# Optimization experiments

Measured on AMD Instinct MI355X. Metric: run time of the kernel, lower is better.

Reference implementation:

```python
import jax, jax.numpy as jnp
import numpy as np
from jax import lax

SEQ_LEN = 256
BATCH = 512
N_INPUTS = 3
N_LAYERS = 2
HIDDEN = 512
TD_ACT = SEQ_LEN  # required: fc1 is Linear(seq_len, 20) applied to td output
N_OUTPUTS = 2


def _lstm_layer(x, h0, c0, Wih, Whh, bih, bhh):
    # x: [S, B, I]; h0, c0: [B, H]; Wih: [4H, I]; Whh: [4H, H]
    def step(carry, xt):
        h, c = carry
        gates = xt @ Wih.T + bih + h @ Whh.T + bhh  # [B, 4H]
        i, f, g, o = jnp.split(gates, 4, axis=-1)
        i = jax.nn.sigmoid(i)
        f = jax.nn.sigmoid(f)
        g = jnp.tanh(g)
        o = jax.nn.sigmoid(o)
        c = f * c + i * g
        h = o * jnp.tanh(c)
        return (h, c), h

    (hT, cT), ys = lax.scan(step, (h0, c0), x)
    return ys, hT, cT


def setup_inputs() -> dict:
    key = jax.random.key(0)
    ks = jax.random.split(key, 16)
    s = 1.0 / np.sqrt(HIDDEN)
    u = lambda k, shape: jax.random.uniform(k, shape, jnp.float32, -s, s)
    return {
        "x": jax.random.normal(ks[0], (SEQ_LEN, BATCH, N_INPUTS), jnp.float32),
        "h0": jax.random.normal(ks[1], (N_LAYERS, BATCH, HIDDEN), jnp.float32),
        "c0": jax.random.normal(ks[2], (N_LAYERS, BATCH, HIDDEN), jnp.float32),
        "Wih0": u(ks[3], (4 * HIDDEN, N_INPUTS)),
        "Whh0": u(ks[4], (4 * HIDDEN, HIDDEN)),
        "bih0": u(ks[5], (4 * HIDDEN,)),
        "bhh0": u(ks[6], (4 * HIDDEN,)),
        "Wih1": u(ks[7], (4 * HIDDEN, HIDDEN)),
        "Whh1": u(ks[8], (4 * HIDDEN, HIDDEN)),
        "bih1": u(ks[9], (4 * HIDDEN,)),
        "bhh1": u(ks[10], (4 * HIDDEN,)),
        "Wtd": u(ks[11], (TD_ACT, 2 * HIDDEN)),
        "btd": u(ks[12], (TD_ACT,)),
        "Wfc1": u(ks[13], (20, SEQ_LEN)),
        "bfc1": jnp.zeros((20,), jnp.float32),
        "Wfc2": u(ks[14], (N_OUTPUTS, 20)),
        "bfc2": jnp.zeros((N_OUTPUTS,), jnp.float32),
    }


def reference(x, h0, c0, Wih0, Whh0, bih0, bhh0, Wih1, Whh1, bih1, bhh1,
              Wtd, btd, Wfc1, bfc1, Wfc2, bfc2):
    # layer 0
    y0, h0T, _ = _lstm_layer(x, h0[0], c0[0], Wih0, Whh0, bih0, bhh0)
    # layer 1
    y1, h1T, _ = _lstm_layer(y0, h0[1], c0[1], Wih1, Whh1, bih1, bhh1)
    # hn[-2] = h0T, hn[-1] = h1T
    cat = jnp.concatenate([h0T, h1T], axis=1)  # [B, 2H]
    td = cat @ Wtd.T + btd                     # [B, TD_ACT == SEQ_LEN]
    fc1 = jax.nn.relu(td @ Wfc1.T + bfc1)      # [B, 20] (dropout p=0 is identity)
    out = fc1 @ Wfc2.T + bfc2                  # [B, 2]
    return out
```

## Files before the change

kernel.cpp:

```cpp
#include <hip/hip_runtime.h>
#include <math.h>

#define BB 512
#define HH 512
#define SS 256
#define XD0 3
#define TDN 256
#define FC1N 20
#define OUTN 2
#define TM 32
#define TN 32
#define TK 32
#define NBLK 256

typedef __attribute__((ext_vector_type(8))) short short8;
typedef __attribute__((ext_vector_type(4))) short short4v;
typedef __attribute__((ext_vector_type(4))) float f32x4;
typedef unsigned long long u64;

__device__ __forceinline__ unsigned short bf16_rne(float f) {
    unsigned u = __float_as_uint(f);
    u += 0x7FFFu + ((u >> 16) & 1u);
    return (unsigned short)(u >> 16);
}
__device__ __forceinline__ float bf16_to_f(unsigned short h) {
    return __uint_as_float(((unsigned)h) << 16);
}
__device__ __forceinline__ float sigmoid_(float x) { return 1.0f / (1.0f + __expf(-x)); }
__device__ __forceinline__ float tanh_(float x) {
    float e = __expf(2.0f * x);
    return 1.0f - 2.0f / (e + 1.0f);
}

__device__ __forceinline__ short8 cload8(const short* p) {
    u64 a = __hip_atomic_load((const u64*)p,     __ATOMIC_RELAXED, __HIP_MEMORY_SCOPE_AGENT);
    u64 b = __hip_atomic_load((const u64*)p + 1, __ATOMIC_RELAXED, __HIP_MEMORY_SCOPE_AGENT);
    union { u64 q[2]; short8 v; } u;
    u.q[0] = a; u.q[1] = b;
    return u.v;
}
__device__ __forceinline__ void cstore4(short* p, short4v v) {
    u64 q; __builtin_memcpy(&q, &v, 8);
    __hip_atomic_store((u64*)p, q, __ATOMIC_RELAXED, __HIP_MEMORY_SCOPE_AGENT);
}

__global__ __launch_bounds__(256)
void cvt_wfrag(const float* __restrict__ W, short* __restrict__ hi, short* __restrict__ lo)
{
    int idx = blockIdx.x * 256 + threadIdx.x;
    int l   = idx & 63;
    int kt  = (idx >> 6) & 15;
    int g   = (idx >> 10) & 3;
    int jt  = idx >> 12;
    int row = g * HH + jt * 16 + (l & 15);
    int col = kt * 32 + (l >> 4) * 8;
    size_t src = (size_t)row * HH + col;
    size_t dst = (size_t)idx * 8;
    #pragma unroll
    for (int e = 0; e < 8; ++e) {
        float v = W[src + e];
        unsigned short h = bf16_rne(v);
        hi[dst + e] = (short)h;
        lo[dst + e] = (short)bf16_rne(v - bf16_to_f(h));
    }
}

__global__ __launch_bounds__(256)
void cvt_hfrag(const float* __restrict__ Hsrc, short* __restrict__ hi, short* __restrict__ lo)
{
    int idx = blockIdx.x * 256 + threadIdx.x;
    int l  = idx & 63;
    int kt = (idx >> 6) & 15;
    int rt = idx >> 10;
    int r = rt * 16 + (l & 15);
    int k = kt * 32 + (l >> 4) * 8;
    size_t src = (size_t)r * HH + k;
    size_t dst = (size_t)idx * 8;
    #pragma unroll
    for (int e = 0; e < 8; ++e) {
        float v = Hsrc[src + e];
        unsigned short h = bf16_rne(v);
        hi[dst + e] = (short)h;
        lo[dst + e] = (short)bf16_rne(v - bf16_to_f(h));
    }
}

__global__ void zero_sync(unsigned* s) { s[threadIdx.x] = 0u; }

__device__ __forceinline__ void grid_barrier(unsigned* sync, int p, int bid)
{
    __syncthreads();
    if (threadIdx.x == 0) {
        const int g = bid & 7;
        unsigned a = __hip_atomic_fetch_add(&sync[g * 32], 1u,
                        __ATOMIC_RELAXED, __HIP_MEMORY_SCOPE_AGENT);
        if (a == (unsigned)((NBLK / 8) * (p + 1) - 1)) {
            unsigned r = __hip_atomic_fetch_add(&sync[256], 1u,
                            __ATOMIC_RELAXED, __HIP_MEMORY_SCOPE_AGENT);
            if (r == (unsigned)(8 * (p + 1) - 1)) {
                __hip_atomic_store(&sync[320], (unsigned)(p + 1),
                                   __ATOMIC_RELAXED, __HIP_MEMORY_SCOPE_AGENT);
            }
        }
        while (__hip_atomic_load(&sync[320], __ATOMIC_RELAXED,
                                 __HIP_MEMORY_SCOPE_AGENT) < (unsigned)(p + 1)) {
            __builtin_amdgcn_s_sleep(2);
        }
    }
    __syncthreads();
}

template<int LAYER>
__device__ __forceinline__ void reduce_epilogue(
    f32x4 (&acc)[4][4], float (*quad)[4096],
    int kh, int l, int tid, int jt, int rblk, int p,
    const float* __restrict__ sbias,
    const float* __restrict__ swin,
    const float* __restrict__ cinit,
    f32x4& cstate,
    short* __restrict__ hfh, short* __restrict__ hfl,
    float* __restrict__ Hf,
    const float* __restrict__ x)
{
    if (kh >= 4) {
        #pragma unroll
        for (int rt = 0; rt < 4; ++rt)
            #pragma unroll
            for (int g = 0; g < 4; ++g)
                #pragma unroll
                for (int q = 0; q < 4; ++q)
                    quad[kh - 4][(g*64 + rt*16 + (l>>4)*4 + q)*16 + (l&15)] = acc[rt][g][q];
    }
    __syncthreads();
    if (kh < 4) {
        #pragma unroll
        for (int rt = 0; rt < 4; ++rt)
            #pragma unroll
            for (int g = 0; g < 4; ++g)
                #pragma unroll
                for (int q = 0; q < 4; ++q)
                    acc[rt][g][q] += quad[kh][(g*64 + rt*16 + (l>>4)*4 + q)*16 + (l&15)];
    }
    __syncthreads();
    if (kh == 2 || kh == 3) {
        #pragma unroll
        for (int rt = 0; rt < 4; ++rt)
            #pragma unroll
            for (int g = 0; g < 4; ++g)
                #pragma unroll
                for (int q = 0; q < 4; ++q)
                    quad[kh][(g*64 + rt*16 + (l>>4)*4 + q)*16 + (l&15)] = acc[rt][g][q];
    }
    __syncthreads();
    if (kh == 0 || kh == 1) {
        #pragma unroll
        for (int rt = 0; rt < 4; ++rt)
            #pragma unroll
            for (int g = 0; g < 4; ++g)
                #pragma unroll
                for (int q = 0; q < 4; ++q)
                    acc[rt][g][q] += quad[kh + 2][(g*64 + rt*16 + (l>>4)*4 + q)*16 + (l&15)];
        if (kh == 1) {
            #pragma unroll
            for (int rt = 0; rt < 4; ++rt)
                #pragma unroll
                for (int g = 0; g < 4; ++g)
                    #pragma unroll
                    for (int q = 0; q < 4; ++q)
                        quad[1][(g*64 + rt*16 + (l>>4)*4 + q)*16 + (l&15)] = acc[rt][g][q];
        }
    }
    __syncthreads();
    if (kh == 0) {
        #pragma unroll
        for (int rt = 0; rt < 4; ++rt)
            #pragma unroll
            for (int g = 0; g < 4; ++g) {
                #pragma unroll
                for (int q = 0; q < 4; ++q) {
                    acc[rt][g][q] += quad[1][(g*64 + rt*16 + (l>>4)*4 + q)*16 + (l&15)];
                    quad[0][(g*64 + rt*16 + (l>>4)*4 + q)*16 + (l&15)] = acc[rt][g][q];
                }
            }
    }
    __syncthreads();

    if (tid < 256) {
        const int rl = tid >> 2;
        const int jl = (tid & 3) * 4;
        const int r  = rblk * 64 + rl;
        const int j  = jt * 16 + jl;
        f32x4 gv[4];
        #pragma unroll
        for (int g = 0; g < 4; ++g) {
            gv[g] = *(const f32x4*)&quad[0][(g*64 + rl)*16 + jl];
            f32x4 bv = *(const f32x4*)&sbias[g*16 + jl];
            #pragma unroll
            for (int q = 0; q < 4; ++q) gv[g][q] += bv[q];
        }
        if (LAYER == 0) {
            const float x0 = x[(size_t)p * BB * XD0 + r * XD0 + 0];
            const float x1 = x[(size_t)p * BB * XD0 + r * XD0 + 1];
            const float x2 = x[(size_t)p * BB * XD0 + r * XD0 + 2];
            #pragma unroll
            for (int g = 0; g < 4; ++g)
                #pragma unroll
                for (int e = 0; e < 4; ++e) {
                    const float* wr_ = &swin[(g*16 + jl + e) * 3];
                    gv[g][e] += x0 * wr_[0] + x1 * wr_[1] + x2 * wr_[2];
                }
        }
        f32x4 cv = cstate;
        if (cinit != nullptr) cv = *(const f32x4*)&cinit[(size_t)r * HH + j];
        float hn[4];
        #pragma unroll
        for (int e = 0; e < 4; ++e) {
            float I = sigmoid_(gv[0][e]);
            float F = sigmoid_(gv[1][e]);
            float G = tanh_(gv[2][e]);
            float O = sigmoid_(gv[3][e]);
            float cn = F * cv[e] + I * G;
            cv[e] = cn;
            hn[e] = O * tanh_(cn);
        }
        cstate = cv;
        const int ktj   = j >> 5;
        const int lanew = (r & 15) | (((j & 31) >> 3) << 4);
        const int e0    = j & 7;
        const int rtg   = r >> 4;
        size_t hoff = ((((size_t)rtg)*16 + ktj)*64 + lanew)*8 + e0;
        short4v hhi, hlo;
        #pragma unroll
        for (int e = 0; e < 4; ++e) {
            unsigned short hb = bf16_rne(hn[e]);
            hhi[e] = (short)hb;
            hlo[e] = (short)bf16_rne(hn[e] - bf16_to_f(hb));
        }
        cstore4(&hfh[hoff], hhi);
        cstore4(&hfl[hoff], hlo);
        if (Hf != nullptr) {
            f32x4 hv;
            #pragma unroll
            for (int e = 0; e < 4; ++e) hv[e] = hn[e];
            *(f32x4*)&Hf[(size_t)r * HH + j] = hv;
        }
    }
    __syncthreads();
}

__global__ __launch_bounds__(512, 2)
void lstm_persist(
    const short* __restrict__ W0h, const short* __restrict__ W0l,
    const short* __restrict__ W1h, const short* __restrict__ W1l,
    const short* __restrict__ WIh, const short* __restrict__ WIl,
    const float* __restrict__ Wih0, const float* __restrict__ x,
    const float* __restrict__ bih0, const float* __restrict__ bhh0,
    const float* __restrict__ bih1, const float* __restrict__ bhh1,
    const float* __restrict__ c0in,
    short* __restrict__ h0fh0, short* __restrict__ h0fl0,
    short* __restrict__ h0fh1, short* __restrict__ h0fl1,
    short* __restrict__ h1fh0, short* __restrict__ h1fl0,
    short* __restrict__ h1fh1, short* __restrict__ h1fl1,
    float* __restrict__ H0f, float* __restrict__ H1f,
    unsigned* __restrict__ sync)
{
    __shared__ float quad[4][4096];
    __shared__ __align__(16) float sb[2][64];
    __shared__ float swin[192];

    const int tid  = threadIdx.x;
    const int kh   = tid >> 6;
    const int l    = tid & 63;
    const int bid  = blockIdx.x;
    const int jt   = bid & 31;
    const int rblk = bid >> 5;

    if (tid < 128) {
        const int L = tid >> 6;
        const int gj = tid & 63;
        const int g = gj >> 4, jl = gj & 15;
        const int j = jt * 16 + jl;
        const float* bi = L ? bih1 : bih0;
        const float* bh = L ? bhh1 : bhh0;
        sb[L][gj] = bi[g * HH + j] + bh[g * HH + j];
    } else if (tid < 320) {
        const int q = tid - 128;
        const int gj = q / 3, d = q - gj * 3;
        const int g = gj >> 4, jl = gj & 15;
        const int j = jt * 16 + jl;
        swin[q] = Wih0[(size_t)(g * HH + j) * XD0 + d];
    }

    short8 b0h[2][4];
    short8 b1h[4][4];
    #pragma unroll
    for (int kk = 0; kk < 2; ++kk)
        #pragma unroll
        for (int g = 0; g < 4; ++g)
            b0h[kk][g] = *(const short8*)&W0h[((((size_t)jt*4 + g)*16 + (kh + kk*8))*64 + l)*8];
    #pragma unroll
    for (int kk = 0; kk < 4; ++kk)
        #pragma unroll
        for (int g = 0; g < 4; ++g) {
            const short* Wh = (kk < 2) ? W1h : WIh;
            const int kt = kh + (kk & 1) * 8;
            b1h[kk][g] = *(const short8*)&Wh[((((size_t)jt*4 + g)*16 + kt)*64 + l)*8];
        }

    f32x4 c0reg, c1reg;
    #pragma unroll
    for (int e = 0; e < 4; ++e) { c0reg[e] = 0.0f; c1reg[e] = 0.0f; }

    __syncthreads();

    for (int p = 0; p <= SS; ++p) {
        const int par = p & 1;
        if (p < SS) {
            const short* Ah = par ? h0fh1 : h0fh0;
            const short* Al = par ? h0fl1 : h0fl0;
            f32x4 acc[4][4];
            #pragma unroll
            for (int rt = 0; rt < 4; ++rt)
                #pragma unroll
                for (int g = 0; g < 4; ++g)
                    #pragma unroll
                    for (int q = 0; q < 4; ++q) acc[rt][g][q] = 0.0f;
            #pragma unroll
            for (int kk = 0; kk < 2; ++kk) {
                const int kt = kh + kk * 8;
                short8 bl[4];
                #pragma unroll
                for (int g = 0; g < 4; ++g)
                    bl[g] = *(const short8*)&W0l[((((size_t)jt*4 + g)*16 + kt)*64 + l)*8];
                #pragma unroll
                for (int rt = 0; rt < 4; ++rt) {
                    const size_t ab = ((((size_t)(rblk*4 + rt))*16 + kt)*64 + l)*8;
                    short8 ah = cload8(&Ah[ab]);
                    short8 al = cload8(&Al[ab]);
                    #pragma unroll
                    for (int g = 0; g < 4; ++g) {
                        acc[rt][g] = __builtin_amdgcn_mfma_f32_16x16x32_bf16(ah, b0h[kk][g], acc[rt][g], 0,0,0);
                        acc[rt][g] = __builtin_amdgcn_mfma_f32_16x16x32_bf16(ah, bl[g],      acc[rt][g], 0,0,0);
                        acc[rt][g] = __builtin_amdgcn_mfma_f32_16x16x32_bf16(al, b0h[kk][g], acc[rt][g], 0,0,0);
                    }
                }
            }
            reduce_epilogue<0>(acc, quad, kh, l, tid, jt, rblk, p,
                               sb[0], swin,
                               (p == 0) ? c0in : nullptr, c0reg,
                               par ? h0fh0 : h0fh1, par ? h0fl0 : h0fl1,
                               (p == SS - 1) ? H0f : nullptr, x);
        }
        if (p >= 1) {
            const short* A1h = par ? h1fh1 : h1fh0;
            const short* A1l = par ? h1fl1 : h1fl0;
            const short* Y0h = par ? h0fh1 : h0fh0;
            const short* Y0l = par ? h0fl1 : h0fl0;
            f32x4 acc[4][4];
            #pragma unroll
            for (int rt = 0; rt < 4; ++rt)
                #pragma unroll
                for (int g = 0; g < 4; ++g)
                    #pragma unroll
                    for (int q = 0; q < 4; ++q) acc[rt][g][q] = 0.0f;
            #pragma unroll
            for (int kk = 0; kk < 4; ++kk) {
                const int kt = kh + (kk & 1) * 8;
                const short* Ah = (kk < 2) ? A1h : Y0h;
                const short* Al = (kk < 2) ? A1l : Y0l;
                const short* Wl = (kk < 2) ? W1l : WIl;
                short8 bl[4];
                #pragma unroll
                for (int g = 0; g < 4; ++g)
                    bl[g] = *(const short8*)&Wl[((((size_t)jt*4 + g)*16 + kt)*64 + l)*8];
                #pragma unroll
                for (int rt = 0; rt < 4; ++rt) {
                    const size_t ab = ((((size_t)(rblk*4 + rt))*16 + kt)*64 + l)*8;
                    short8 ah = cload8(&Ah[ab]);
                    short8 al = cload8(&Al[ab]);
                    #pragma unroll
                    for (int g = 0; g < 4; ++g) {
                        acc[rt][g] = __builtin_amdgcn_mfma_f32_16x16x32_bf16(ah, b1h[kk][g], acc[rt][g], 0,0,0);
                        acc[rt][g] = __builtin_amdgcn_mfma_f32_16x16x32_bf16(ah, bl[g],      acc[rt][g], 0,0,0);
                        acc[rt][g] = __builtin_amdgcn_mfma_f32_16x16x32_bf16(al, b1h[kk][g], acc[rt][g], 0,0,0);
                    }
                }
            }
            reduce_epilogue<1>(acc, quad, kh, l, tid, jt, rblk, p,
                               sb[1], swin,
                               (p == 1) ? (c0in + (size_t)BB*HH) : nullptr, c1reg,
                               par ? h1fh0 : h1fh1, par ? h1fl0 : h1fl1,
                               (p == SS) ? H1f : nullptr, x);
        }
        grid_barrier(sync, p, bid);
    }
}

__global__ __launch_bounds__(256)
void td_kernel(const float* __restrict__ h0T, const float* __restrict__ h1T,
               const float* __restrict__ Wtd, const float* __restrict__ btd,
               float* __restrict__ td)
{
    __shared__ float a_lds[TM][TK + 1];
    __shared__ float b_lds[TN][TK + 1];
    const int t = threadIdx.x;
    const int nl = t & 31;
    const int mq = t >> 5;
    const int n0 = blockIdx.x * TN;
    const int m0 = blockIdx.y * TM;
    float acc[4] = {0.f, 0.f, 0.f, 0.f};

    for (int k0 = 0; k0 < 2 * HH; k0 += TK) {
        const float* src = (k0 < HH) ? h0T : h1T;
        int kb = k0 & (HH - 1);
        #pragma unroll
        for (int i = 0; i < (TM * TK) / 256; ++i) {
            int idx = t + i * 256;
            int r = idx >> 5, kk = idx & 31;
            a_lds[r][kk] = src[(size_t)(m0 + r) * HH + kb + kk];
        }
        #pragma unroll
        for (int i = 0; i < (TN * TK) / 256; ++i) {
            int idx = t + i * 256;
            int jn = idx >> 5, kk = idx & 31;
            b_lds[jn][kk] = Wtd[(size_t)(n0 + jn) * (2 * HH) + k0 + kk];
        }
        __syncthreads();
        #pragma unroll
        for (int kk = 0; kk < TK; ++kk) {
            float bv = b_lds[nl][kk];
            #pragma unroll
            for (int rr = 0; rr < 4; ++rr)
                acc[rr] = fmaf(a_lds[mq * 4 + rr][kk], bv, acc[rr]);
        }
        __syncthreads();
    }
    #pragma unroll
    for (int rr = 0; rr < 4; ++rr)
        td[(size_t)(m0 + mq * 4 + rr) * TDN + n0 + nl] = acc[rr] + btd[n0 + nl];
}

__global__ __launch_bounds__(256)
void fc_kernel(const float* __restrict__ td,
               const float* __restrict__ Wfc1, const float* __restrict__ bfc1,
               const float* __restrict__ Wfc2, const float* __restrict__ bfc2,
               float* __restrict__ out)
{
    __shared__ float td_lds[32][TDN];
    __shared__ float f1_lds[32][FC1N];
    const int t = threadIdx.x;
    const int r0 = blockIdx.x * 32;

    #pragma unroll
    for (int i = 0; i < (32 * TDN) / 256; ++i) {
        int idx = t + i * 256;
        int r = idx >> 8, k = idx & 255;
        td_lds[r][k] = td[(size_t)(r0 + r) * TDN + k];
    }
    __syncthreads();

    for (int idx = t; idx < 32 * FC1N; idx += 256) {
        int r = idx / FC1N, o = idx % FC1N;
        float s = bfc1[o];
        for (int k = 0; k < TDN; ++k) s = fmaf(td_lds[r][k], Wfc1[o * TDN + k], s);
        f1_lds[r][o] = fmaxf(s, 0.0f);
    }
    __syncthreads();

    for (int idx = t; idx < 32 * OUTN; idx += 256) {
        int r = idx / OUTN, o = idx % OUTN;
        float s = bfc2[o];
        for (int k = 0; k < FC1N; ++k) s = fmaf(f1_lds[r][k], Wfc2[o * FC1N + k], s);
        out[(size_t)(r0 + r) * OUTN + o] = s;
    }
}

extern "C" void kernel_launch(void* const* d_in, const int* in_sizes, int n_in,
                              void* d_out, int out_size, void* d_ws, size_t ws_size,
                              hipStream_t stream)
{
    const float* x    = (const float*)d_in[0];
    const float* h0   = (const float*)d_in[1];
    const float* c0   = (const float*)d_in[2];
    const float* Wih0 = (const float*)d_in[3];
    const float* Whh0 = (const float*)d_in[4];
    const float* bih0 = (const float*)d_in[5];
    const float* bhh0 = (const float*)d_in[6];
    const float* Wih1 = (const float*)d_in[7];
    const float* Whh1 = (const float*)d_in[8];
    const float* bih1 = (const float*)d_in[9];
    const float* bhh1 = (const float*)d_in[10];
    const float* Wtd  = (const float*)d_in[11];
    const float* btd  = (const float*)d_in[12];
    const float* Wfc1 = (const float*)d_in[13];
    const float* bfc1 = (const float*)d_in[14];
    const float* Wfc2 = (const float*)d_in[15];
    const float* bfc2 = (const float*)d_in[16];
    float* out = (float*)d_out;

    const size_t WSZ = (size_t)4 * HH * HH;
    const size_t HFR = (size_t)32 * 16 * 64 * 8;
    const size_t HSZ = (size_t)BB * HH;

    char* pp = (char*)d_ws;
    short* W0h = (short*)pp; pp += WSZ * 2;
    short* W0l = (short*)pp; pp += WSZ * 2;
    short* W1h = (short*)pp; pp += WSZ * 2;
    short* W1l = (short*)pp; pp += WSZ * 2;
    short* WIh = (short*)pp; pp += WSZ * 2;
    short* WIl = (short*)pp; pp += WSZ * 2;
    short* h0fh0 = (short*)pp; pp += HFR * 2;
    short* h0fl0 = (short*)pp; pp += HFR * 2;
    short* h0fh1 = (short*)pp; pp += HFR * 2;
    short* h0fl1 = (short*)pp; pp += HFR * 2;
    short* h1fh0 = (short*)pp; pp += HFR * 2;
    short* h1fl0 = (short*)pp; pp += HFR * 2;
    short* h1fh1 = (short*)pp; pp += HFR * 2;
    short* h1fl1 = (short*)pp; pp += HFR * 2;
    float* H0f = (float*)pp; pp += HSZ * 4;
    float* H1f = (float*)pp; pp += HSZ * 4;
    float* TD  = (float*)pp; pp += (size_t)BB * TDN * 4;
    unsigned* sync = (unsigned*)pp; pp += 512 * 4;

    cvt_wfrag<<<dim3(512), dim3(256), 0, stream>>>(Whh0, W0h, W0l);
    cvt_wfrag<<<dim3(512), dim3(256), 0, stream>>>(Whh1, W1h, W1l);
    cvt_wfrag<<<dim3(512), dim3(256), 0, stream>>>(Wih1, WIh, WIl);
    cvt_hfrag<<<dim3(128), dim3(256), 0, stream>>>(h0,        h0fh0, h0fl0);
    cvt_hfrag<<<dim3(128), dim3(256), 0, stream>>>(h0 + HSZ,  h1fh1, h1fl1);
    zero_sync<<<dim3(1), dim3(512), 0, stream>>>(sync);

    lstm_persist<<<dim3(NBLK), dim3(512), 0, stream>>>(
        W0h, W0l, W1h, W1l, WIh, WIl,
        Wih0, x, bih0, bhh0, bih1, bhh1, c0,
        h0fh0, h0fl0, h0fh1, h0fl1,
        h1fh0, h1fl0, h1fh1, h1fl1,
        H0f, H1f, sync);

    const dim3 gtd(TDN / TN, BB / TM);
    td_kernel<<<gtd, dim3(256), 0, stream>>>(H0f, H1f, Wtd, btd, TD);
    fc_kernel<<<dim3(BB / 32), dim3(256), 0, stream>>>(TD, Wfc1, bfc1, Wfc2, bfc2, out);

    (void)in_sizes; (void)n_in; (void)out_size; (void)ws_size;
}
```

Baseline: 9.958 ms.

## Map row blocks to XCDs and use per-XCD barriers with non-coherent loads

At launch each block reads its hardware XCD id and takes a slot on that XCD. If every XCD holds exactly 32 blocks, each XCD owns one batch row block (rblk = xcd). Those blocks then sync only with the 32 blocks on their own XCD and exchange h fragments with plain cached loads and stores instead of agent-scope atomics. This is meant to replace the device-wide barrier and cross-XCD coherent traffic with a cheaper local barrier and L2-resident data. It relies on same-XCD L2 coherence for the plain accesses, and falls back to the old global path if the placement check fails.

```diff
diff --git a/kernel.cpp b/kernel.cpp
--- a/kernel.cpp
+++ b/kernel.cpp
@@ -18,6 +18,8 @@
 typedef __attribute__((ext_vector_type(4))) float f32x4;
 typedef unsigned long long u64;
 
+#define SYNC_WORDS 1024
+
 __device__ __forceinline__ unsigned short bf16_rne(float f) {
     unsigned u = __float_as_uint(f);
     u += 0x7FFFu + ((u >> 16) & 1u);
@@ -42,6 +44,15 @@
 __device__ __forceinline__ void cstore4(short* p, short4v v) {
     u64 q; __builtin_memcpy(&q, &v, 8);
     __hip_atomic_store((u64*)p, q, __ATOMIC_RELAXED, __HIP_MEMORY_SCOPE_AGENT);
+}
+
+template<bool COH> __device__ __forceinline__ short8 ald(const short* p) {
+    if constexpr (COH) return cload8(p);
+    else return *(const short8*)p;
+}
+template<bool COH> __device__ __forceinline__ void ast(short* p, short4v v) {
+    if constexpr (COH) cstore4(p, v);
+    else *(short4v*)p = v;
 }
 
 __global__ __launch_bounds__(256)
@@ -85,42 +96,55 @@
     }
 }
 
-__global__ void zero_sync(unsigned* s) { s[threadIdx.x] = 0u; }
-
-__device__ __forceinline__ void grid_barrier(unsigned* sync, int p, int bid)
+__global__ void zero_sync(unsigned* s) { s[blockIdx.x * 256 + threadIdx.x] = 0u; }
+
+template<bool COH>
+__device__ __forceinline__ void phase_barrier(unsigned* sync, int p, int bid, int rblk)
 {
     __syncthreads();
     if (threadIdx.x == 0) {
-        const int g = bid & 7;
-        unsigned a = __hip_atomic_fetch_add(&sync[g * 32], 1u,
-                        __ATOMIC_RELAXED, __HIP_MEMORY_SCOPE_AGENT);
-        if (a == (unsigned)((NBLK / 8) * (p + 1) - 1)) {
-            unsigned r = __hip_atomic_fetch_add(&sync[256], 1u,
+        if constexpr (COH) {
+            const int g = bid & 7;
+            unsigned a = __hip_atomic_fetch_add(&sync[g * 32], 1u,
                             __ATOMIC_RELAXED, __HIP_MEMORY_SCOPE_AGENT);
-            if (r == (unsigned)(8 * (p + 1) - 1)) {
-                __hip_atomic_store(&sync[320], (unsigned)(p + 1),
+            if (a == (unsigned)((NBLK / 8) * (p + 1) - 1)) {
+                unsigned r = __hip_atomic_fetch_add(&sync[256], 1u,
+                                __ATOMIC_RELAXED, __HIP_MEMORY_SCOPE_AGENT);
+                if (r == (unsigned)(8 * (p + 1) - 1)) {
+                    __hip_atomic_store(&sync[320], (unsigned)(p + 1),
+                                       __ATOMIC_RELAXED, __HIP_MEMORY_SCOPE_AGENT);
+                }
+            }
+            while (__hip_atomic_load(&sync[320], __ATOMIC_RELAXED,
+                                     __HIP_MEMORY_SCOPE_AGENT) < (unsigned)(p + 1)) {
+                __builtin_amdgcn_s_sleep(2);
+            }
+        } else {
+            unsigned* cnt = &sync[512 + rblk * 64];
+            unsigned* gen = &sync[512 + rblk * 64 + 32];
+            unsigned a = __hip_atomic_fetch_add(cnt, 1u,
+                            __ATOMIC_RELAXED, __HIP_MEMORY_SCOPE_AGENT);
+            if (a == (unsigned)(32 * (p + 1) - 1)) {
+                __hip_atomic_store(gen, (unsigned)(p + 1),
                                    __ATOMIC_RELAXED, __HIP_MEMORY_SCOPE_AGENT);
             }
-        }
-        while (__hip_atomic_load(&sync[320], __ATOMIC_RELAXED,
-                                 __HIP_MEMORY_SCOPE_AGENT) < (unsigned)(p + 1)) {
-            __builtin_amdgcn_s_sleep(2);
-        }
-    }
-    __syncthreads();
-}
-
-template<int LAYER>
+            while (__hip_atomic_load(gen, __ATOMIC_RELAXED,
+                                     __HIP_MEMORY_SCOPE_AGENT) < (unsigned)(p + 1)) {
+                __builtin_amdgcn_s_sleep(1);
+            }
+        }
+    }
+    __syncthreads();
+}
+
+template<int LAYER, bool COH>
 __device__ __forceinline__ void reduce_epilogue(
     f32x4 (&acc)[4][4], float (*quad)[4096],
     int kh, int l, int tid, int jt, int rblk, int p,
-    const float* __restrict__ sbias,
-    const float* __restrict__ swin,
-    const float* __restrict__ cinit,
-    f32x4& cstate,
+    const float* __restrict__ sbias, const float* __restrict__ swin,
+    const float* __restrict__ cinit, f32x4& cstate,
     short* __restrict__ hfh, short* __restrict__ hfl,
-    float* __restrict__ Hf,
-    const float* __restrict__ x)
+    float* __restrict__ Hf, const float* __restrict__ x)
 {
     if (kh >= 4) {
         #pragma unroll
@@ -236,8 +260,8 @@
             hhi[e] = (short)hb;
             hlo[e] = (short)bf16_rne(hn[e] - bf16_to_f(hb));
         }
-        cstore4(&hfh[hoff], hhi);
-        cstore4(&hfl[hoff], hlo);
+        ast<COH>(&hfh[hoff], hhi);
+        ast<COH>(&hfl[hoff], hlo);
         if (Hf != nullptr) {
             f32x4 hv;
             #pragma unroll
@@ -246,6 +270,145 @@
         }
     }
     __syncthreads();
+}
+
+template<bool COH>
+__device__ __forceinline__ void run_main(
+    int tid, int bid, int rblk, int jt,
+    float (*quad)[4096], float (*sb)[64], float* swin,
+    const short* W0h, const short* W0l,
+    const short* W1h, const short* W1l,
+    const short* WIh, const short* WIl,
+    const float* Wih0, const float* x,
+    const float* bih0, const float* bhh0,
+    const float* bih1, const float* bhh1,
+    const float* c0in,
+    short* h0fh0, short* h0fl0, short* h0fh1, short* h0fl1,
+    short* h1fh0, short* h1fl0, short* h1fh1, short* h1fl1,
+    float* H0f, float* H1f, unsigned* sync)
+{
+    const int kh = tid >> 6;
+    const int l  = tid & 63;
+
+    if (tid < 128) {
+        const int L = tid >> 6;
+        const int gj = tid & 63;
+        const int g = gj >> 4, jl = gj & 15;
+        const int j = jt * 16 + jl;
+        const float* bi = L ? bih1 : bih0;
+        const float* bh = L ? bhh1 : bhh0;
+        sb[L][gj] = bi[g * HH + j] + bh[g * HH + j];
+    } else if (tid < 320) {
+        const int q = tid - 128;
+        const int gj = q / 3, d = q - gj * 3;
+        const int g = gj >> 4, jl = gj & 15;
+        const int j = jt * 16 + jl;
+        swin[q] = Wih0[(size_t)(g * HH + j) * XD0 + d];
+    }
+
+    short8 b0h[2][4];
+    short8 b1h[4][4];
+    #pragma unroll
+    for (int kk = 0; kk < 2; ++kk)
+        #pragma unroll
+        for (int g = 0; g < 4; ++g)
+            b0h[kk][g] = *(const short8*)&W0h[((((size_t)jt*4 + g)*16 + (kh + kk*8))*64 + l)*8];
+    #pragma unroll
+    for (int kk = 0; kk < 4; ++kk)
+        #pragma unroll
+        for (int g = 0; g < 4; ++g) {
+            const short* Wh = (kk < 2) ? W1h : WIh;
+            const int kt = kh + (kk & 1) * 8;
+            b1h[kk][g] = *(const short8*)&Wh[((((size_t)jt*4 + g)*16 + kt)*64 + l)*8];
+        }
+
+    f32x4 c0reg, c1reg;
+    #pragma unroll
+    for (int e = 0; e < 4; ++e) { c0reg[e] = 0.0f; c1reg[e] = 0.0f; }
+
+    __syncthreads();
+
+    for (int p = 0; p <= SS; ++p) {
+        const int par = p & 1;
+        if (p < SS) {
+            const short* Ah = par ? h0fh1 : h0fh0;
+            const short* Al = par ? h0fl1 : h0fl0;
+            f32x4 acc[4][4];
+            #pragma unroll
+            for (int rt = 0; rt < 4; ++rt)
+                #pragma unroll
+                for (int g = 0; g < 4; ++g)
+                    #pragma unroll
+                    for (int q = 0; q < 4; ++q) acc[rt][g][q] = 0.0f;
+            #pragma unroll
+            for (int kk = 0; kk < 2; ++kk) {
+                const int kt = kh + kk * 8;
+                short8 bl[4];
+                #pragma unroll
+                for (int g = 0; g < 4; ++g)
+                    bl[g] = *(const short8*)&W0l[((((size_t)jt*4 + g)*16 + kt)*64 + l)*8];
+                #pragma unroll
+                for (int rt = 0; rt < 4; ++rt) {
+                    const size_t ab = ((((size_t)(rblk*4 + rt))*16 + kt)*64 + l)*8;
+                    short8 ah = ald<COH>(&Ah[ab]);
+                    short8 al = ald<COH>(&Al[ab]);
+                    #pragma unroll
+                    for (int g = 0; g < 4; ++g) {
+                        acc[rt][g] = __builtin_amdgcn_mfma_f32_16x16x32_bf16(ah, b0h[kk][g], acc[rt][g], 0,0,0);
+                        acc[rt][g] = __builtin_amdgcn_mfma_f32_16x16x32_bf16(ah, bl[g],      acc[rt][g], 0,0,0);
+                        acc[rt][g] = __builtin_amdgcn_mfma_f32_16x16x32_bf16(al, b0h[kk][g], acc[rt][g], 0,0,0);
+                    }
+                }
+            }
+            reduce_epilogue<0, COH>(acc, quad, kh, l, tid, jt, rblk, p,
+                               sb[0], swin,
+                               (p == 0) ? c0in : nullptr, c0reg,
+                               par ? h0fh0 : h0fh1, par ? h0fl0 : h0fl1,
+                               (p == SS - 1) ? H0f : nullptr, x);
+        }
+        if (p >= 1) {
+            const short* A1h = par ? h1fh1 : h1fh0;
+            const short* A1l = par ? h1fl1 : h1fl0;
+            const short* Y0h = par ? h0fh1 : h0fh0;
+            const short* Y0l = par ? h0fl1 : h0fl0;
+            f32x4 acc[4][4];
+            #pragma unroll
+            for (int rt = 0; rt < 4; ++rt)
+                #pragma unroll
+                for (int g = 0; g < 4; ++g)
+                    #pragma unroll
+                    for (int q = 0; q < 4; ++q) acc[rt][g][q] = 0.0f;
+            #pragma unroll
+            for (int kk = 0; kk < 4; ++kk) {
+                const int kt = kh + (kk & 1) * 8;
+                const short* Ah = (kk < 2) ? A1h : Y0h;
+                const short* Al = (kk < 2) ? A1l : Y0l;
+                const short* Wl = (kk < 2) ? W1l : WIl;
+                short8 bl[4];
+                #pragma unroll
+                for (int g = 0; g < 4; ++g)
+                    bl[g] = *(const short8*)&Wl[((((size_t)jt*4 + g)*16 + kt)*64 + l)*8];
+                #pragma unroll
+                for (int rt = 0; rt < 4; ++rt) {
+                    const size_t ab = ((((size_t)(rblk*4 + rt))*16 + kt)*64 + l)*8;
+                    short8 ah = ald<COH>(&Ah[ab]);
+                    short8 al = ald<COH>(&Al[ab]);
+                    #pragma unroll
+                    for (int g = 0; g < 4; ++g) {
+                        acc[rt][g] = __builtin_amdgcn_mfma_f32_16x16x32_bf16(ah, b1h[kk][g], acc[rt][g], 0,0,0);
+                        acc[rt][g] = __builtin_amdgcn_mfma_f32_16x16x32_bf16(ah, bl[g],      acc[rt][g], 0,0,0);
+                        acc[rt][g] = __builtin_amdgcn_mfma_f32_16x16x32_bf16(al, b1h[kk][g], acc[rt][g], 0,0,0);
+                    }
+                }
+            }
+            reduce_epilogue<1, COH>(acc, quad, kh, l, tid, jt, rblk, p,
+                               sb[1], swin,
+                               (p == 1) ? (c0in + (size_t)BB*HH) : nullptr, c1reg,
+                               par ? h1fh0 : h1fh1, par ? h1fl0 : h1fl1,
+                               (p == SS) ? H1f : nullptr, x);
+        }
+        phase_barrier<COH>(sync, p, bid, rblk);
+    }
 }
 
 __global__ __launch_bounds__(512, 2)
@@ -267,132 +430,49 @@
     __shared__ float quad[4][4096];
     __shared__ __align__(16) float sb[2][64];
     __shared__ float swin[192];
-
-    const int tid  = threadIdx.x;
-    const int kh   = tid >> 6;
-    const int l    = tid & 63;
-    const int bid  = blockIdx.x;
-    const int jt   = bid & 31;
-    const int rblk = bid >> 5;
-
-    if (tid < 128) {
-        const int L = tid >> 6;
-        const int gj = tid & 63;
-        const int g = gj >> 4, jl = gj & 15;
-        const int j = jt * 16 + jl;
-        const float* bi = L ? bih1 : bih0;
-        const float* bh = L ? bhh1 : bhh0;
-        sb[L][gj] = bi[g * HH + j] + bh[g * HH + j];
-    } else if (tid < 320) {
-        const int q = tid - 128;
-        const int gj = q / 3, d = q - gj * 3;
-        const int g = gj >> 4, jl = gj & 15;
-        const int j = jt * 16 + jl;
-        swin[q] = Wih0[(size_t)(g * HH + j) * XD0 + d];
-    }
-
-    short8 b0h[2][4];
-    short8 b1h[4][4];
-    #pragma unroll
-    for (int kk = 0; kk < 2; ++kk)
-        #pragma unroll
-        for (int g = 0; g < 4; ++g)
-            b0h[kk][g] = *(const short8*)&W0h[((((size_t)jt*4 + g)*16 + (kh + kk*8))*64 + l)*8];
-    #pragma unroll
-    for (int kk = 0; kk < 4; ++kk)
-        #pragma unroll
-        for (int g = 0; g < 4; ++g) {
-            const short* Wh = (kk < 2) ? W1h : WIh;
-            const int kt = kh + (kk & 1) * 8;
-            b1h[kk][g] = *(const short8*)&Wh[((((size_t)jt*4 + g)*16 + kt)*64 + l)*8];
-        }
-
-    f32x4 c0reg, c1reg;
-    #pragma unroll
-    for (int e = 0; e < 4; ++e) { c0reg[e] = 0.0f; c1reg[e] = 0.0f; }
-
-    __syncthreads();
-
-    for (int p = 0; p <= SS; ++p) {
-        const int par = p & 1;
-        if (p < SS) {
-            const short* Ah = par ? h0fh1 : h0fh0;
-            const short* Al = par ? h0fl1 : h0fl0;
-            f32x4 acc[4][4];
-            #pragma unroll
-            for (int rt = 0; rt < 4; ++rt)
-                #pragma unroll
-                for (int g = 0; g < 4; ++g)
-                    #pragma unroll
-                    for (int q = 0; q < 4; ++q) acc[rt][g][q] = 0.0f;
-            #pragma unroll
-            for (int kk = 0; kk < 2; ++kk) {
-                const int kt = kh + kk * 8;
-                short8 bl[4];
-                #pragma unroll
-                for (int g = 0; g < 4; ++g)
-                    bl[g] = *(const short8*)&W0l[((((size_t)jt*4 + g)*16 + kt)*64 + l)*8];
-                #pragma unroll
-                for (int rt = 0; rt < 4; ++rt) {
-                    const size_t ab = ((((size_t)(rblk*4 + rt))*16 + kt)*64 + l)*8;
-                    short8 ah = cload8(&Ah[ab]);
-                    short8 al = cload8(&Al[ab]);
-                    #pragma unroll
-                    for (int g = 0; g < 4; ++g) {
-                        acc[rt][g] = __builtin_amdgcn_mfma_f32_16x16x32_bf16(ah, b0h[kk][g], acc[rt][g], 0,0,0);
-                        acc[rt][g] = __builtin_amdgcn_mfma_f32_16x16x32_bf16(ah, bl[g],      acc[rt][g], 0,0,0);
-                        acc[rt][g] = __builtin_amdgcn_mfma_f32_16x16x32_bf16(al, b0h[kk][g], acc[rt][g], 0,0,0);
-                    }
-                }
-            }
-            reduce_epilogue<0>(acc, quad, kh, l, tid, jt, rblk, p,
-                               sb[0], swin,
-                               (p == 0) ? c0in : nullptr, c0reg,
-                               par ? h0fh0 : h0fh1, par ? h0fl0 : h0fl1,
-                               (p == SS - 1) ? H0f : nullptr, x);
-        }
-        if (p >= 1) {
-            const short* A1h = par ? h1fh1 : h1fh0;
-            const short* A1l = par ? h1fl1 : h1fl0;
-            const short* Y0h = par ? h0fh1 : h0fh0;
-            const short* Y0l = par ? h0fl1 : h0fl0;
-            f32x4 acc[4][4];
-            #pragma unroll
-            for (int rt = 0; rt < 4; ++rt)
-                #pragma unroll
-                for (int g = 0; g < 4; ++g)
-                    #pragma unroll
-                    for (int q = 0; q < 4; ++q) acc[rt][g][q] = 0.0f;
-            #pragma unroll
-            for (int kk = 0; kk < 4; ++kk) {
-                const int kt = kh + (kk & 1) * 8;
-                const short* Ah = (kk < 2) ? A1h : Y0h;
-                const short* Al = (kk < 2) ? A1l : Y0l;
-                const short* Wl = (kk < 2) ? W1l : WIl;
-                short8 bl[4];
-                #pragma unroll
-                for (int g = 0; g < 4; ++g)
-                    bl[g] = *(const short8*)&Wl[((((size_t)jt*4 + g)*16 + kt)*64 + l)*8];
-                #pragma unroll
-                for (int rt = 0; rt < 4; ++rt) {
-                    const size_t ab = ((((size_t)(rblk*4 + rt))*16 + kt)*64 + l)*8;
-                    short8 ah = cload8(&Ah[ab]);
-                    short8 al = cload8(&Al[ab]);
-                    #pragma unroll
-                    for (int g = 0; g < 4; ++g) {
-                        acc[rt][g] = __builtin_amdgcn_mfma_f32_16x16x32_bf16(ah, b1h[kk][g], acc[rt][g], 0,0,0);
-                        acc[rt][g] = __builtin_amdgcn_mfma_f32_16x16x32_bf16(ah, bl[g],      acc[rt][g], 0,0,0);
-                        acc[rt][g] = __builtin_amdgcn_mfma_f32_16x16x32_bf16(al, b1h[kk][g], acc[rt][g], 0,0,0);
-                    }
-                }
-            }
-            reduce_epilogue<1>(acc, quad, kh, l, tid, jt, rblk, p,
-                               sb[1], swin,
-                               (p == 1) ? (c0in + (size_t)BB*HH) : nullptr, c1reg,
-                               par ? h1fh0 : h1fh1, par ? h1fl0 : h1fl1,
-                               (p == SS) ? H1f : nullptr, x);
-        }
-        grid_barrier(sync, p, bid);
+    __shared__ unsigned info[2];
+
+    const int tid = threadIdx.x;
+    const int bid = blockIdx.x;
+
+    if (tid == 0) {
+        unsigned xcd;
+        asm volatile("s_getreg_b32 %0, hwreg(20, 0, 4)" : "=s"(xcd));
+        xcd &= 7u;
+        unsigned slot = __hip_atomic_fetch_add(&sync[384 + xcd], 1u,
+                          __ATOMIC_RELAXED, __HIP_MEMORY_SCOPE_AGENT);
+        unsigned a = __hip_atomic_fetch_add(&sync[416], 1u,
+                          __ATOMIC_RELAXED, __HIP_MEMORY_SCOPE_AGENT);
+        if (a == (unsigned)(NBLK - 1))
+            __hip_atomic_store(&sync[448], 1u, __ATOMIC_RELAXED, __HIP_MEMORY_SCOPE_AGENT);
+        while (__hip_atomic_load(&sync[448], __ATOMIC_RELAXED,
+                                 __HIP_MEMORY_SCOPE_AGENT) < 1u)
+            __builtin_amdgcn_s_sleep(2);
+        bool good = (slot < 32u);
+        #pragma unroll
+        for (int xx = 0; xx < 8; ++xx)
+            good = good && (__hip_atomic_load(&sync[384 + xx], __ATOMIC_RELAXED,
+                                              __HIP_MEMORY_SCOPE_AGENT) == 32u);
+        info[0] = good ? (0x100u | xcd) : 0u;
+        info[1] = slot;
+    }
+    __syncthreads();
+    const bool good = (info[0] & 0x100u) != 0u;
+    const int rblk = good ? (int)(info[0] & 7u) : (bid >> 5);
+    const int jt   = good ? (int)info[1]        : (bid & 31);
+
+    if (good) {
+        run_main<false>(tid, bid, rblk, jt, quad, sb, swin,
+            W0h, W0l, W1h, W1l, WIh, WIl, Wih0, x,
+            bih0, bhh0, bih1, bhh1, c0in,
+            h0fh0, h0fl0, h0fh1, h0fl1, h1fh0, h1fl0, h1fh1, h1fl1,
+            H0f, H1f, sync);
+    } else {
+        run_main<true>(tid, bid, rblk, jt, quad, sb, swin,
+            W0h, W0l, W1h, W1l, WIh, WIl, Wih0, x,
+            bih0, bhh0, bih1, bhh1, c0in,
+            h0fh0, h0fl0, h0fh1, h0fl1, h1fh0, h1fl0, h1fh1, h1fl1,
+            H0f, H1f, sync);
     }
 }
 
@@ -520,14 +600,14 @@
     float* H0f = (float*)pp; pp += HSZ * 4;
     float* H1f = (float*)pp; pp += HSZ * 4;
     float* TD  = (float*)pp; pp += (size_t)BB * TDN * 4;
-    unsigned* sync = (unsigned*)pp; pp += 512 * 4;
+    unsigned* sync = (unsigned*)pp; pp += SYNC_WORDS * 4;
 
     cvt_wfrag<<<dim3(512), dim3(256), 0, stream>>>(Whh0, W0h, W0l);
     cvt_wfrag<<<dim3(512), dim3(256), 0, stream>>>(Whh1, W1h, W1l);
     cvt_wfrag<<<dim3(512), dim3(256), 0, stream>>>(Wih1, WIh, WIl);
     cvt_hfrag<<<dim3(128), dim3(256), 0, stream>>>(h0,        h0fh0, h0fl0);
     cvt_hfrag<<<dim3(128), dim3(256), 0, stream>>>(h0 + HSZ,  h1fh1, h1fl1);
-    zero_sync<<<dim3(1), dim3(512), 0, stream>>>(sync);
+    zero_sync<<<dim3(SYNC_WORDS / 256), dim3(256), 0, stream>>>(sync);
 
     lstm_persist<<<dim3(NBLK), dim3(512), 0, stream>>>(
         W0h, W0l, W1h, W1l, WIh, WIl,
```

Measured after the change: 9.291 ms. -6.7%, faster.
